# Kernel tuning notes

Hardware: AMD Instinct MI355X
Metric: run time of the kernel (lower is better)

The kernel has to match this reference:

```python
import jax, jax.numpy as jnp
import numpy as np

NH, NKV, HD = 8, 1, 256
EPS = 1e-6
SCALE = 1.0 / np.sqrt(HD)


def _rmsnorm(x, w, eps=EPS):
    # Gemma-style: normalize in fp32, scale by raw weight
    xf = x.astype(jnp.float32)
    rms = jax.lax.rsqrt(jnp.mean(xf * xf, axis=-1, keepdims=True) + eps)
    return (xf * rms).astype(x.dtype) * w


def _apply_rope(q, cos, sin):
    # q: (B, H, T, D); cos/sin: (T, D/2)
    half = q.shape[-1] // 2
    q1, q2 = q[..., :half], q[..., half:]
    c = cos[None, None, :, :]
    s = sin[None, None, :, :]
    return jnp.concatenate([q1 * c - q2 * s, q2 * c + q1 * s], axis=-1)


def setup_inputs() -> dict:
    key = jax.random.key(0)
    ks = jax.random.split(key, 8)
    B, T, H = 2, 2048, 1536
    MAXPOS, HALF = 4096, HD // 2
    x = jax.random.normal(ks[0], (B, T, H), dtype=jnp.float32)
    positions = jnp.arange(T, dtype=jnp.int64) if jax.config.jax_enable_x64 else jnp.arange(T, dtype=jnp.int32)
    # real RoPE tables
    inv_freq = 1.0 / (10000.0 ** (np.arange(0, HALF, dtype=np.float32) / HALF))
    ang = np.arange(MAXPOS, dtype=np.float32)[:, None] * inv_freq[None, :]
    cos = jnp.asarray(np.cos(ang))
    sin = jnp.asarray(np.sin(ang))
    # additive causal mask: 0 on/below diag, -1e9 above
    causal_mask = jnp.where(jnp.tril(jnp.ones((T, T), dtype=bool)), 0.0, -1e9).astype(jnp.float32)
    sc = 0.02
    Wq = jax.random.normal(ks[1], (H, NH * HD), dtype=jnp.float32) * sc
    Wk = jax.random.normal(ks[2], (H, NKV * HD), dtype=jnp.float32) * sc
    Wv = jax.random.normal(ks[3], (H, NKV * HD), dtype=jnp.float32) * sc
    Wo = jax.random.normal(ks[4], (NH * HD, H), dtype=jnp.float32) * sc
    q_norm_w = jnp.ones((HD,), dtype=jnp.float32)
    k_norm_w = jnp.ones((HD,), dtype=jnp.float32)
    return {"x": x, "positions": positions, "cos": cos, "sin": sin,
            "causal_mask": causal_mask, "Wq": Wq, "Wk": Wk, "Wv": Wv,
            "Wo": Wo, "q_norm_w": q_norm_w, "k_norm_w": k_norm_w}


def reference(x, positions, cos, sin, causal_mask, Wq, Wk, Wv, Wo, q_norm_w, k_norm_w):
    B, T, _ = x.shape
    q = (x @ Wq).reshape(B, T, NH, HD)
    k = (x @ Wk).reshape(B, T, NKV, HD)
    v = (x @ Wv).reshape(B, T, NKV, HD)
    q = _rmsnorm(q, q_norm_w)
    k = _rmsnorm(k, k_norm_w)
    q = q.transpose(0, 2, 1, 3)  # (B, NH, T, HD)
    k = k.transpose(0, 2, 1, 3)  # (B, NKV, T, HD)
    v = v.transpose(0, 2, 1, 3)
    cos_pos = cos[positions]
    sin_pos = sin[positions]
    q = _apply_rope(q, cos_pos, sin_pos)
    k = _apply_rope(k, cos_pos, sin_pos)
    if NH != NKV:
        n_rep = NH // NKV
        k = jnp.repeat(k, n_rep, axis=1)
        v = jnp.repeat(v, n_rep, axis=1)
    attn = jnp.einsum('bhqd,bhkd->bhqk', q, k) * SCALE
    attn = attn + causal_mask[None, None]
    attn = jax.nn.softmax(attn, axis=-1)
    out = jnp.einsum('bhqk,bhkd->bhqd', attn, v)
    out = out.transpose(0, 2, 1, 3).reshape(B, T, NH * HD)
    return out @ Wo
```

## Files before the change

kernel.cpp:

```cpp
#include <hip/hip_runtime.h>
#include <hip/hip_bf16.h>

typedef __bf16 bf16x8 __attribute__((ext_vector_type(8)));
typedef float  f32x4  __attribute__((ext_vector_type(4)));

__device__ __forceinline__ f32x4 mfma16(bf16x8 a, bf16x8 b, f32x4 c) {
    return __builtin_amdgcn_mfma_f32_16x16x32_bf16(a, b, c, 0, 0, 0);
}

__device__ __forceinline__ void gload_lds16(const void* g, void* l) {
    __builtin_amdgcn_global_load_lds(
        (const __attribute__((address_space(1))) void*)g,
        (__attribute__((address_space(3))) void*)l, 16, 0, 0);
}

__device__ __forceinline__ float bf2f(unsigned short u) {
    unsigned int x = (unsigned int)u << 16;
    return __builtin_bit_cast(float, x);
}
__device__ __forceinline__ unsigned short f2bf(float f) {
    return __builtin_bit_cast(unsigned short, __float2bfloat16(f));
}

#define B_   2
#define T_   2048
#define H_   1536
#define NH_  8
#define HD_  256
#define ND_  2048
#define NQKV 2560

__global__ __launch_bounds__(256) void cvt_f32_bf16(
        const float* __restrict__ src, __hip_bfloat16* __restrict__ dst, int n8) {
    int i = blockIdx.x * 256 + threadIdx.x;
    if (i >= n8) return;
    const float4* s4 = reinterpret_cast<const float4*>(src) + (size_t)i * 2;
    float4 a = s4[0], b = s4[1];
    short4 o0, o1;
    o0.x = (short)f2bf(a.x); o0.y = (short)f2bf(a.y);
    o0.z = (short)f2bf(a.z); o0.w = (short)f2bf(a.w);
    o1.x = (short)f2bf(b.x); o1.y = (short)f2bf(b.y);
    o1.z = (short)f2bf(b.z); o1.w = (short)f2bf(b.w);
    short4* d4 = reinterpret_cast<short4*>(dst) + (size_t)i * 2;
    d4[0] = o0; d4[1] = o1;
}

__global__ __launch_bounds__(256) void transpose_f32_bf16(
        const float* __restrict__ src, __hip_bfloat16* __restrict__ dst,
        int R, int C) {
    __shared__ float tile[32][33];
    int c0 = blockIdx.x * 32, r0 = blockIdx.y * 32;
    int tx = threadIdx.x & 31, ty = threadIdx.x >> 5;
#pragma unroll
    for (int i = 0; i < 32; i += 8)
        tile[ty + i][tx] = src[(size_t)(r0 + ty + i) * C + c0 + tx];
    __syncthreads();
#pragma unroll
    for (int i = 0; i < 32; i += 8)
        dst[(size_t)(c0 + ty + i) * R + r0 + tx] = __float2bfloat16(tile[tx][ty + i]);
}

__global__ __launch_bounds__(256) void transpose_bf16_s(
        const __hip_bfloat16* __restrict__ src, __hip_bfloat16* __restrict__ dst,
        int R, int C, int ss) {
    __shared__ __hip_bfloat16 tile[32][33];
    int c0 = blockIdx.x * 32, r0 = blockIdx.y * 32;
    int tx = threadIdx.x & 31, ty = threadIdx.x >> 5;
#pragma unroll
    for (int i = 0; i < 32; i += 8)
        tile[ty + i][tx] = src[(size_t)(r0 + ty + i) * ss + c0 + tx];
    __syncthreads();
#pragma unroll
    for (int i = 0; i < 32; i += 8)
        dst[(size_t)(c0 + ty + i) * R + r0 + tx] = tile[tx][ty + i];
}

template <bool F32OUT>
__global__ __launch_bounds__(256) void gemm_bt(
        const __hip_bfloat16* __restrict__ A, const __hip_bfloat16* __restrict__ Bt,
        void* __restrict__ Cp, int M, int N, int K) {
    __shared__ char smem[16384];
    char* As = smem;
    char* Bs = smem + 8192;
    const int tid  = threadIdx.x;
    const int lane = tid & 63;
    const int w    = tid >> 6;
    const int wm   = w >> 1, wn = w & 1;
    const int m0   = blockIdx.y * 128, n0 = blockIdx.x * 128;

    f32x4 acc[4][4] = {};

    for (int k0 = 0; k0 < K; k0 += 32) {
#pragma unroll
        for (int it = 0; it < 2; ++it) {
            int o   = it * 4096 + tid * 16;
            int row = o >> 6;
            int cb  = (o & 63) ^ (((o >> 7) & 3) << 4);
            gload_lds16(A  + (size_t)(m0 + row) * K + k0 + (cb >> 1),
                        As + it * 4096 + w * 1024);
            gload_lds16(Bt + (size_t)(n0 + row) * K + k0 + (cb >> 1),
                        Bs + it * 4096 + w * 1024);
        }
        __syncthreads();

        bf16x8 af[4], bfr[4];
#pragma unroll
        for (int i = 0; i < 4; ++i) {
            int ar = wm * 64 + i * 16 + (lane & 15);
            int q  = ar * 64 + ((lane >> 4) << 4);
            af[i]  = *(const bf16x8*)(As + (q ^ (((q >> 7) & 3) << 4)));
            int br = wn * 64 + i * 16 + (lane & 15);
            int p  = br * 64 + ((lane >> 4) << 4);
            bfr[i] = *(const bf16x8*)(Bs + (p ^ (((p >> 7) & 3) << 4)));
        }
#pragma unroll
        for (int i = 0; i < 4; ++i)
#pragma unroll
            for (int j = 0; j < 4; ++j)
                acc[i][j] = mfma16(af[i], bfr[j], acc[i][j]);
        __syncthreads();
    }

#pragma unroll
    for (int i = 0; i < 4; ++i) {
        int rbase = m0 + wm * 64 + i * 16 + ((lane >> 4) << 2);
#pragma unroll
        for (int j = 0; j < 4; ++j) {
            int col = n0 + wn * 64 + j * 16 + (lane & 15);
#pragma unroll
            for (int r = 0; r < 4; ++r) {
                if (F32OUT)
                    ((float*)Cp)[(size_t)(rbase + r) * N + col] = acc[i][j][r];
                else
                    ((__hip_bfloat16*)Cp)[(size_t)(rbase + r) * N + col] =
                        __float2bfloat16(acc[i][j][r]);
            }
        }
    }
}

__global__ __launch_bounds__(256) void norm_rope(
        const __hip_bfloat16* __restrict__ QKV,
        const float* __restrict__ cosT, const float* __restrict__ sinT,
        const int* __restrict__ positions,
        const float* __restrict__ qw, const float* __restrict__ kw,
        __hip_bfloat16* __restrict__ Qn, __hip_bfloat16* __restrict__ Kn) {
    int gw   = blockIdx.x * 4 + (threadIdx.x >> 6);
    int lane = threadIdx.x & 63;
    int bt   = gw / 9;
    int r    = gw - bt * 9;
    int b    = bt >> 11, t = bt & 2047;

    const __hip_bfloat16* src = QKV + (size_t)bt * NQKV + (r < 8 ? r * HD_ : ND_);
    const float* w;
    __hip_bfloat16* dst;
    float sc;
    if (r < 8) {
        w   = qw;
        dst = Qn + (((size_t)(b * NH_ + r) * T_) + t) * HD_;
        sc  = 0.0901684400555590f;
    } else {
        w   = kw;
        dst = Kn + (size_t)bt * HD_;
        sc  = 1.0f;
    }

    short4 raw = *reinterpret_cast<const short4*>(src + lane * 4);
    float v[4];
    v[0] = bf2f((unsigned short)raw.x); v[1] = bf2f((unsigned short)raw.y);
    v[2] = bf2f((unsigned short)raw.z); v[3] = bf2f((unsigned short)raw.w);

    float ss = v[0]*v[0] + v[1]*v[1] + v[2]*v[2] + v[3]*v[3];
#pragma unroll
    for (int d = 1; d < 64; d <<= 1) ss += __shfl_xor(ss, d);
    float rms = rsqrtf(ss * (1.0f / HD_) + 1e-6f);

    int pos = positions[t];
    float4 c4 = *reinterpret_cast<const float4*>(cosT + (size_t)pos * 128 + (lane & 31) * 4);
    float4 s4 = *reinterpret_cast<const float4*>(sinT + (size_t)pos * 128 + (lane & 31) * 4);
    float cv[4] = { c4.x, c4.y, c4.z, c4.w };
    float sv[4] = { s4.x, s4.y, s4.z, s4.w };

    float4 w4 = *reinterpret_cast<const float4*>(w + lane * 4);
    float wv[4] = { w4.x, w4.y, w4.z, w4.w };

    float nf[4], out[4];
#pragma unroll
    for (int j = 0; j < 4; ++j) nf[j] = v[j] * rms * wv[j];
#pragma unroll
    for (int j = 0; j < 4; ++j) {
        float pf = __shfl_xor(nf[j], 32);
        out[j] = (lane < 32) ? (nf[j] * cv[j] - pf * sv[j])
                             : (nf[j] * cv[j] + pf * sv[j]);
    }
    short4 o4;
    o4.x = (short)f2bf(out[0] * sc); o4.y = (short)f2bf(out[1] * sc);
    o4.z = (short)f2bf(out[2] * sc); o4.w = (short)f2bf(out[3] * sc);
    *reinterpret_cast<short4*>(dst + lane * 4) = o4;
}

#define NPAIR 80
__global__ __launch_bounds__(256) void flash_attn_split(
        const __hip_bfloat16* __restrict__ Qn, const __hip_bfloat16* __restrict__ Kn,
        const __hip_bfloat16* __restrict__ Vt,
        __hip_bfloat16* __restrict__ Opart, float* __restrict__ ml) {
    __shared__ char smem[2 * 16384 + 2 * 16384 + 4 * 1536];
    char* Ps = smem + 65536;

    const int tid = threadIdx.x, lane = tid & 63, wid = tid >> 6;
    const int p = blockIdx.x, bh = blockIdx.y;
    const int b = bh >> 3;

    int qt, c;
    if (p < 8)       { qt = p;                c = 0; }
    else if (p < 24) { qt = 8 + ((p - 8) >> 1);  c = (p - 8) & 1; }
    else if (p < 48) { qt = 16 + (p - 24) / 3;   c = (p - 24) % 3; }
    else             { qt = 24 + ((p - 48) >> 2); c = (p - 48) & 3; }

    const int kv0 = c * 512;
    const int kv1 = min(kv0 + 512, (qt + 1) * 64);
    const int q0  = qt * 64 + wid * 16;
    const int nst = (kv1 - kv0) >> 5;

    const __hip_bfloat16* Qbase = Qn + ((size_t)bh * T_ + q0) * HD_;
    const __hip_bfloat16* Kb    = Kn + (size_t)b * T_ * HD_;
    const __hip_bfloat16* Vb    = Vt + (size_t)b * HD_ * T_;

    bf16x8 qf[8];
#pragma unroll
    for (int ks = 0; ks < 8; ++ks)
        qf[ks] = *(const bf16x8*)(Qbase + (size_t)(lane & 15) * HD_ + ks * 32 +
                                  ((lane >> 4) << 3));

    bf16x8 onesf;
    {
        __bf16 one = (__bf16)1.0f, zro = (__bf16)0.0f;
        __bf16 val = ((lane & 15) == 0) ? one : zro;
#pragma unroll
        for (int i = 0; i < 8; ++i) onesf[i] = val;
    }

    f32x4 acc[16] = {};
    f32x4 accl = {};

    auto STAGE = [&](int bsel, int kbb) {
        char* Kd = smem + bsel * 16384;
        char* Vd = smem + 32768 + bsel * 16384;
#pragma unroll
        for (int it = 0; it < 4; ++it) {
            int o = it * 4096 + tid * 16;
            {
                int row = o >> 9;
                int cb  = (o & 511) ^ ((row & 31) << 4);
                gload_lds16(Kb + (size_t)(kbb + row) * HD_ + (cb >> 1),
                            Kd + it * 4096 + wid * 1024);
            }
            {
                int row = o >> 6;
                int cb  = (o & 63) ^ (((o >> 7) & 3) << 4);
                gload_lds16(Vb + (size_t)row * T_ + kbb + (cb >> 1),
                            Vd + it * 4096 + wid * 1024);
            }
        }
    };

    STAGE(0, kv0);
    __syncthreads();

    for (int i = 0; i < nst; ++i) {
        const int kb = kv0 + (i << 5);
        if (i + 1 < nst) STAGE((i + 1) & 1, kb + 32);

        const char* Ksb = smem + (i & 1) * 16384;
        const char* Vsb = smem + 32768 + (i & 1) * 16384;

        f32x4 s[2] = {};
#pragma unroll
        for (int cf = 0; cf < 2; ++cf) {
#pragma unroll
            for (int ks = 0; ks < 8; ++ks) {
                int krow = cf * 16 + (lane & 15);
                int q    = krow * 512 + ks * 64 + ((lane >> 4) << 4);
                int sw   = q ^ (((q >> 9) & 31) << 4);
                bf16x8 kf = *(const bf16x8*)(Ksb + sw);
                s[cf] = mfma16(qf[ks], kf, s[cf]);
            }
        }

        const bool nm = (kb + 31 > q0);
        __hip_bfloat16* pw = (__hip_bfloat16*)(Ps + wid * 1536);
#pragma unroll
        for (int r = 0; r < 4; ++r) {
            int rw = ((lane >> 4) << 2) + r;
            float s0 = s[0][r], s1 = s[1][r];
            if (nm) {
                int qrow = q0 + rw;
                if (kb + (lane & 15) > qrow)      s0 = -1e30f;
                if (kb + 16 + (lane & 15) > qrow) s1 = -1e30f;
            }
            pw[rw * 48 + (lane & 15)]      = __float2bfloat16(exp2f(s0));
            pw[rw * 48 + 16 + (lane & 15)] = __float2bfloat16(exp2f(s1));
        }

        bf16x8 pf = *(const bf16x8*)(Ps + wid * 1536 + (lane & 15) * 96 +
                                     ((lane >> 4) << 4));
        accl = mfma16(pf, onesf, accl);
#pragma unroll
        for (int nf = 0; nf < 16; ++nf) {
            int vrow = nf * 16 + (lane & 15);
            int q    = vrow * 64 + ((lane >> 4) << 4);
            int sw   = q ^ (((q >> 7) & 3) << 4);
            bf16x8 vf = *(const bf16x8*)(Vsb + sw);
            acc[nf] = mfma16(pf, vf, acc[nf]);
        }

        if (i + 1 < nst) __syncthreads();
    }

    const int slot = bh * NPAIR + p;
    __hip_bfloat16* ob = Opart + (size_t)slot * (64 * 256);
#pragma unroll
    for (int r = 0; r < 4; ++r) {
        int rw = wid * 16 + ((lane >> 4) << 2) + r;
        __hip_bfloat16* orow = ob + (size_t)rw * 256;
#pragma unroll
        for (int nf = 0; nf < 16; ++nf)
            orow[nf * 16 + (lane & 15)] = __float2bfloat16(acc[nf][r]);
        if ((lane & 15) == 0) ml[slot * 64 + rw] = accl[r];
    }
}

__global__ __launch_bounds__(256) void attn_combine(
        const __hip_bfloat16* __restrict__ Opart, const float* __restrict__ ml,
        __hip_bfloat16* __restrict__ Obuf) {
    const int bid = blockIdx.x;
    const int bh = bid >> 5, qt = bid & 31;
    const int b = bh >> 3, h = bh & 7;

    int ps, np;
    if (qt < 8)       { ps = qt;                 np = 1; }
    else if (qt < 16) { ps = 8 + 2 * (qt - 8);   np = 2; }
    else if (qt < 24) { ps = 24 + 3 * (qt - 16); np = 3; }
    else              { ps = 48 + 4 * (qt - 24); np = 4; }
    const int slot0 = bh * NPAIR + ps;

    const int t = threadIdx.x;
    const int row = t >> 2, quad = t & 3;

    float L = 0.0f;
    for (int i = 0; i < np; ++i) L += ml[(slot0 + i) * 64 + row];
    float rL = 1.0f / L;

    __hip_bfloat16* orow = Obuf + ((size_t)(b * T_ + qt * 64 + row)) * ND_ +
                           h * HD_ + quad * 64;
#pragma unroll
    for (int cc = 0; cc < 8; ++cc) {
        float a[8] = {0,0,0,0,0,0,0,0};
        for (int i = 0; i < np; ++i) {
            const __hip_bfloat16* pr = Opart + (size_t)(slot0 + i) * (64 * 256) +
                                       (size_t)row * 256 + quad * 64 + cc * 8;
            short4 v0 = *reinterpret_cast<const short4*>(pr);
            short4 v1 = *reinterpret_cast<const short4*>(pr + 4);
            a[0] += bf2f((unsigned short)v0.x);
            a[1] += bf2f((unsigned short)v0.y);
            a[2] += bf2f((unsigned short)v0.z);
            a[3] += bf2f((unsigned short)v0.w);
            a[4] += bf2f((unsigned short)v1.x);
            a[5] += bf2f((unsigned short)v1.y);
            a[6] += bf2f((unsigned short)v1.z);
            a[7] += bf2f((unsigned short)v1.w);
        }
        short4 o0, o1;
        o0.x = (short)f2bf(a[0] * rL); o0.y = (short)f2bf(a[1] * rL);
        o0.z = (short)f2bf(a[2] * rL); o0.w = (short)f2bf(a[3] * rL);
        o1.x = (short)f2bf(a[4] * rL); o1.y = (short)f2bf(a[5] * rL);
        o1.z = (short)f2bf(a[6] * rL); o1.w = (short)f2bf(a[7] * rL);
        *reinterpret_cast<short4*>(orow + cc * 8)     = o0;
        *reinterpret_cast<short4*>(orow + cc * 8 + 4) = o1;
    }
}

extern "C" void kernel_launch(void* const* d_in, const int* in_sizes, int n_in,
                              void* d_out, int out_size, void* d_ws, size_t ws_size,
                              hipStream_t stream) {
    const float* x    = (const float*)d_in[0];
    const int*   pos  = (const int*)d_in[1];
    const float* cosT = (const float*)d_in[2];
    const float* sinT = (const float*)d_in[3];
    const float* Wq = (const float*)d_in[5];
    const float* Wk = (const float*)d_in[6];
    const float* Wv = (const float*)d_in[7];
    const float* Wo = (const float*)d_in[8];
    const float* qw = (const float*)d_in[9];
    const float* kw = (const float*)d_in[10];

    char* ws0 = (char*)d_ws;
    __hip_bfloat16* WqkvT  = (__hip_bfloat16*)(ws0 + 0);
    __hip_bfloat16* xb     = (__hip_bfloat16*)(ws0 + 7864320);
    __hip_bfloat16* QKVraw = (__hip_bfloat16*)(ws0 + 20447232);
    __hip_bfloat16* Opart  = (__hip_bfloat16*)(ws0 + 0);
    float*          ml     = (float*)(ws0 + 41943040);
    __hip_bfloat16* WoT    = (__hip_bfloat16*)(ws0 + 42598400);
    __hip_bfloat16* Qn     = (__hip_bfloat16*)(ws0 + 48889856);
    __hip_bfloat16* Obuf   = Qn;
    __hip_bfloat16* Kn     = (__hip_bfloat16*)(ws0 + 65667072);
    __hip_bfloat16* Vt     = (__hip_bfloat16*)(ws0 + 67764224);
    float* out = (float*)d_out;

    const int MT = B_ * T_;

    cvt_f32_bf16<<<(MT * H_ / 8 + 255) / 256, 256, 0, stream>>>(x, xb, MT * H_ / 8);

    transpose_f32_bf16<<<dim3(ND_ / 32, H_ / 32), 256, 0, stream>>>(
        Wq, WqkvT, H_, ND_);
    transpose_f32_bf16<<<dim3(HD_ / 32, H_ / 32), 256, 0, stream>>>(
        Wk, WqkvT + (size_t)ND_ * H_, H_, HD_);
    transpose_f32_bf16<<<dim3(HD_ / 32, H_ / 32), 256, 0, stream>>>(
        Wv, WqkvT + (size_t)(ND_ + HD_) * H_, H_, HD_);
    transpose_f32_bf16<<<dim3(H_ / 32, ND_ / 32), 256, 0, stream>>>(
        Wo, WoT, ND_, H_);

    gemm_bt<false><<<dim3(NQKV / 128, MT / 128), 256, 0, stream>>>(
        xb, WqkvT, QKVraw, MT, NQKV, H_);

    norm_rope<<<(MT * 9) / 4, 256, 0, stream>>>(
        QKVraw, cosT, sinT, pos, qw, kw, Qn, Kn);

    for (int b = 0; b < B_; ++b)
        transpose_bf16_s<<<dim3(HD_ / 32, T_ / 32), 256, 0, stream>>>(
            QKVraw + (size_t)b * T_ * NQKV + ND_ + HD_,
            Vt + (size_t)b * HD_ * T_, T_, HD_, NQKV);

    flash_attn_split<<<dim3(NPAIR, B_ * NH_), 256, 0, stream>>>(
        Qn, Kn, Vt, Opart, ml);
    attn_combine<<<B_ * NH_ * 32, 256, 0, stream>>>(Opart, ml, Obuf);

    gemm_bt<true><<<dim3(H_ / 128, MT / 128), 256, 0, stream>>>(
        Obuf, WoT, out, MT, H_, ND_);
}
```

Measured before the change: 268.9 us.

## Double-buffer GEMM LDS tiles and use partial vmcnt waits in attention

The GEMM kernel now double-buffers its A/B LDS tiles, issuing the global-to-LDS loads for the next K step before computing on the current one. In both GEMM and attention, the full __syncthreads is replaced with an explicit s_waitcnt vmcnt(N) plus s_barrier, so the wait covers only the older loads while the prefetch keeps running. This aims to overlap global load latency with MFMA work. The cost is doubled GEMM shared memory, which may lower occupancy, and hand-counted vmcnt values that must exactly match the number of outstanding loads per stage.

Measured after the change: 249.9 us. 7.1% less time.

```diff
diff --git a/kernel.cpp b/kernel.cpp
--- a/kernel.cpp
+++ b/kernel.cpp
@@ -79,9 +79,7 @@
 __global__ __launch_bounds__(256) void gemm_bt(
         const __hip_bfloat16* __restrict__ A, const __hip_bfloat16* __restrict__ Bt,
         void* __restrict__ Cp, int M, int N, int K) {
-    __shared__ char smem[16384];
-    char* As = smem;
-    char* Bs = smem + 8192;
+    __shared__ char smem[32768];
     const int tid  = threadIdx.x;
     const int lane = tid & 63;
     const int w    = tid >> 6;
@@ -90,7 +88,9 @@
 
     f32x4 acc[4][4] = {};
 
-    for (int k0 = 0; k0 < K; k0 += 32) {
+    auto STAGE = [&](int bsel, int k0) {
+        char* As = smem + bsel * 16384;
+        char* Bs = As + 8192;
 #pragma unroll
         for (int it = 0; it < 2; ++it) {
             int o   = it * 4096 + tid * 16;
@@ -101,7 +101,22 @@
             gload_lds16(Bt + (size_t)(n0 + row) * K + k0 + (cb >> 1),
                         Bs + it * 4096 + w * 1024);
         }
-        __syncthreads();
+    };
+
+    const int nk = K >> 5;
+    STAGE(0, 0);
+    for (int ik = 0; ik < nk; ++ik) {
+        if (ik + 1 < nk) {
+            STAGE((ik + 1) & 1, (ik + 1) << 5);
+            asm volatile("s_waitcnt vmcnt(4)" ::: "memory");
+        } else {
+            asm volatile("s_waitcnt vmcnt(0)" ::: "memory");
+        }
+        __builtin_amdgcn_s_barrier();
+        __builtin_amdgcn_sched_barrier(0);
+
+        const char* As = smem + (ik & 1) * 16384;
+        const char* Bs = As + 8192;
 
         bf16x8 af[4], bfr[4];
 #pragma unroll
@@ -118,7 +133,8 @@
 #pragma unroll
             for (int j = 0; j < 4; ++j)
                 acc[i][j] = mfma16(af[i], bfr[j], acc[i][j]);
-        __syncthreads();
+
+        if (ik + 1 < nk) __builtin_amdgcn_s_barrier();
     }
 
 #pragma unroll
@@ -265,11 +281,16 @@
     };
 
     STAGE(0, kv0);
-    __syncthreads();
-
     for (int i = 0; i < nst; ++i) {
         const int kb = kv0 + (i << 5);
-        if (i + 1 < nst) STAGE((i + 1) & 1, kb + 32);
+        if (i + 1 < nst) {
+            STAGE((i + 1) & 1, kb + 32);
+            asm volatile("s_waitcnt vmcnt(8)" ::: "memory");
+        } else {
+            asm volatile("s_waitcnt vmcnt(0)" ::: "memory");
+        }
+        __builtin_amdgcn_s_barrier();
+        __builtin_amdgcn_sched_barrier(0);
 
         const char* Ksb = smem + (i & 1) * 16384;
         const char* Vsb = smem + 32768 + (i & 1) * 16384;
@@ -314,7 +335,7 @@
             acc[nf] = mfma16(pf, vf, acc[nf]);
         }
 
-        if (i + 1 < nst) __syncthreads();
+        if (i + 1 < nst) __builtin_amdgcn_s_barrier();
     }
 
     const int slot = bh * NPAIR + p;
```
